# Performance work log

Hardware: AMD Instinct MI355X
Metric: run time of the kernel (lower is better)

The kernel has to match this reference:

```python
import jax, jax.numpy as jnp
import numpy as np

D = 1024
H = 16
HD = D // H
R = 16
EPS = 1e-5


def _ln(x, w, b):
    mu = jnp.mean(x, axis=-1, keepdims=True)
    var = jnp.mean((x - mu) ** 2, axis=-1, keepdims=True)
    return (x - mu) * jax.lax.rsqrt(var + EPS) * w + b


def setup_inputs() -> dict:
    key = jax.random.key(0)
    ks = jax.random.split(key, 8)
    B, N = 32, 257
    s = 0.02
    return {
        "q_x": jax.random.normal(ks[0], (B, N, D), jnp.float32),
        "ln1_w": jnp.ones((D,), jnp.float32),
        "ln1_b": jnp.zeros((D,), jnp.float32),
        "in_proj_w": jax.random.normal(ks[1], (3 * D, D), jnp.float32) * s,
        "in_proj_b": jnp.zeros((3 * D,), jnp.float32),
        "out_w": jax.random.normal(ks[2], (D, D), jnp.float32) * s,
        "out_b": jnp.zeros((D,), jnp.float32),
        "ln2_w": jnp.ones((D,), jnp.float32),
        "ln2_b": jnp.zeros((D,), jnp.float32),
        "fc_w": jax.random.normal(ks[3], (4 * D, D), jnp.float32) * s,
        "fc_b": jnp.zeros((4 * D,), jnp.float32),
        "proj_w": jax.random.normal(ks[4], (D, 4 * D), jnp.float32) * s,
        "proj_b": jnp.zeros((D,), jnp.float32),
    }


def reference(q_x, ln1_w, ln1_b, in_proj_w, in_proj_b, out_w, out_b,
              ln2_w, ln2_b, fc_w, fc_b, proj_w, proj_b):
    B, N, _ = q_x.shape
    # --- attention (no size bias / no padding mask on first call) ---
    h = _ln(q_x, ln1_w, ln1_b)
    qkv = h @ in_proj_w.T + in_proj_b            # [B,N,3D]
    q, k, v = jnp.split(qkv, 3, axis=-1)
    to_heads = lambda t: t.reshape(B, N, H, HD).transpose(0, 2, 1, 3)  # [B,H,N,hd]
    q, k, v = to_heads(q), to_heads(k), to_heads(v)
    metric = k.mean(axis=1)                      # [B,N,hd] ToMe metric
    attn = jax.nn.softmax(jnp.einsum('bhnd,bhmd->bhnm', q, k) / np.sqrt(HD).astype(np.float32), axis=-1)
    o = jnp.einsum('bhnm,bhmd->bhnd', attn, v).transpose(0, 2, 1, 3).reshape(B, N, D)
    x = q_x + (o @ out_w.T + out_b)
    # --- ToMe: bipartite soft matching + weighted-average merge (size=None -> ones) ---
    r = min(R, (N - 1) // 2)                     # class token protected
    m = metric / jnp.linalg.norm(metric, axis=-1, keepdims=True)
    a, bm = m[:, ::2, :], m[:, 1::2, :]          # [B,Na,hd], [B,Nb,hd]
    scores = jnp.einsum('bnd,bmd->bnm', a, bm)
    scores = scores.at[:, 0, :].set(-jnp.inf)    # never merge class token
    node_max = scores.max(axis=-1)               # [B,Na]
    node_idx = scores.argmax(axis=-1)            # [B,Na]
    edge_idx = jnp.argsort(-node_max, axis=-1)   # descending similarity
    unm_idx = jnp.sort(edge_idx[:, r:], axis=-1) # keep order; cls token first
    src_idx = edge_idx[:, :r]
    dst_idx = jnp.take_along_axis(node_idx, src_idx, axis=1)  # [B,r]
    bi = jnp.arange(B)[:, None]

    def merge_sum(t):
        s, d = t[:, ::2], t[:, 1::2]
        unm = jnp.take_along_axis(s, unm_idx[:, :, None], axis=1)
        src = jnp.take_along_axis(s, src_idx[:, :, None], axis=1)
        d = d.at[bi, dst_idx].add(src)
        return jnp.concatenate([unm, d], axis=1)  # [B, N-r, C]

    size = jnp.ones((B, N, 1), x.dtype)
    x = merge_sum(x * size)
    size = merge_sum(size)
    x = x / size
    # --- MLP ---
    h2 = _ln(x, ln2_w, ln2_b)
    h2 = jax.nn.gelu(h2 @ fc_w.T + fc_b, approximate=False)
    x = x + (h2 @ proj_w.T + proj_b)
    return x
```

## Files before the change

kernel.cpp:

```cpp
#include <hip/hip_runtime.h>
#include <math.h>

#define D_ 1024
#define H_ 16
#define HD_ 64
#define BATCH 32
#define NTOK 257
#define NROWS (BATCH*NTOK)
#define NE 129
#define NO 128
#define RR 16
#define UNM 113
#define NMERGED 241
#define MROWS (BATCH*NMERGED)
#define SELSTRIDE 288

typedef unsigned short u16;
typedef unsigned int u32;
typedef __bf16 bf16x8 __attribute__((ext_vector_type(8)));
typedef float floatx4 __attribute__((ext_vector_type(4)));

__device__ __forceinline__ u16 f2bf(float f) {
    u32 u = __float_as_uint(f);
    u += 0x7fffu + ((u >> 16) & 1u);
    return (u16)(u >> 16);
}

__global__ __launch_bounds__(256) void ln_kernel(const float* __restrict__ x,
                                                 const float* __restrict__ w,
                                                 const float* __restrict__ bia,
                                                 float* __restrict__ outf,
                                                 u16* __restrict__ outb) {
    int row = blockIdx.x;
    const float* xr = x + (size_t)row * D_;
    int t = threadIdx.x;
    float v[4];
#pragma unroll
    for (int i = 0; i < 4; i++) v[i] = xr[t + 256 * i];
    float s = v[0] + v[1] + v[2] + v[3];
#pragma unroll
    for (int o = 32; o; o >>= 1) s += __shfl_down(s, o);
    __shared__ float sm[8];
    int wv = t >> 6, ln = t & 63;
    if (ln == 0) sm[wv] = s;
    __syncthreads();
    float mu = (sm[0] + sm[1] + sm[2] + sm[3]) * (1.0f / D_);
    float d0 = v[0] - mu, d1 = v[1] - mu, d2 = v[2] - mu, d3 = v[3] - mu;
    float q = d0 * d0 + d1 * d1 + d2 * d2 + d3 * d3;
#pragma unroll
    for (int o = 32; o; o >>= 1) q += __shfl_down(q, o);
    if (ln == 0) sm[4 + wv] = q;
    __syncthreads();
    float var = (sm[4] + sm[5] + sm[6] + sm[7]) * (1.0f / D_);
    float rs = rsqrtf(var + 1e-5f);
#pragma unroll
    for (int i = 0; i < 4; i++) {
        int c = t + 256 * i;
        float o = (v[i] - mu) * rs * w[c] + bia[c];
        if (outf) outf[(size_t)row * D_ + c] = o;
        outb[(size_t)row * D_ + c] = f2bf(o);
    }
}

__global__ __launch_bounds__(256) void wm_kernel(const float* __restrict__ W,
                                                 const float* __restrict__ bias,
                                                 float* __restrict__ WmT,
                                                 float* __restrict__ bm) {
    int e = blockIdx.x * 256 + threadIdx.x;
    if (e < 64 * 1024) {
        int d = e >> 10, c = e & 1023;
        float s = 0.f;
#pragma unroll
        for (int hh = 0; hh < 16; hh++)
            s += W[(size_t)(1024 + hh * 64 + d) * 1024 + c];
        WmT[(size_t)c * 64 + d] = s * (1.0f / 16.0f);
    }
    if (e < 64) {
        float s = 0.f;
        for (int hh = 0; hh < 16; hh++) s += bias[1024 + hh * 64 + e];
        bm[e] = s * (1.0f / 16.0f);
    }
}

__global__ __launch_bounds__(256) void castw_kernel(const float* __restrict__ s0,
                                                    const float* __restrict__ s1,
                                                    const float* __restrict__ s2,
                                                    const float* __restrict__ s3,
                                                    u16* __restrict__ d0, u16* __restrict__ d1,
                                                    u16* __restrict__ d2, u16* __restrict__ d3) {
    size_t gi = ((size_t)blockIdx.x * 256 + threadIdx.x) * 8;
    const float* s; u16* d; size_t off;
    if (gi < 3145728)        { s = s0; d = d0; off = gi; }
    else if (gi < 4194304)   { s = s1; d = d1; off = gi - 3145728; }
    else if (gi < 8388608)   { s = s2; d = d2; off = gi - 4194304; }
    else                     { s = s3; d = d3; off = gi - 8388608; }
    float4 a = *(const float4*)(s + off);
    float4 b = *(const float4*)(s + off + 4);
    uint4 o;
    o.x = (u32)f2bf(a.x) | ((u32)f2bf(a.y) << 16);
    o.y = (u32)f2bf(a.z) | ((u32)f2bf(a.w) << 16);
    o.z = (u32)f2bf(b.x) | ((u32)f2bf(b.y) << 16);
    o.w = (u32)f2bf(b.z) | ((u32)f2bf(b.w) << 16);
    *(uint4*)(d + off) = o;
}

__global__ __launch_bounds__(256) void metric_kernel(const float* __restrict__ A,
                                                     const float* __restrict__ WmT,
                                                     const float* __restrict__ bm,
                                                     float* __restrict__ metric) {
    int wv = threadIdx.x >> 6, ln = threadIdx.x & 63;
    int row0 = blockIdx.x * 16 + wv * 4;
    const float* a0 = A + (size_t)row0 * 1024;
    float acc0 = 0.f, acc1 = 0.f, acc2 = 0.f, acc3 = 0.f;
    for (int k = 0; k < 1024; k += 8) {
#pragma unroll
        for (int kk = 0; kk < 8; kk++) {
            float w = WmT[(size_t)(k + kk) * 64 + ln];
            acc0 = fmaf(a0[k + kk], w, acc0);
            acc1 = fmaf(a0[1024 + k + kk], w, acc1);
            acc2 = fmaf(a0[2048 + k + kk], w, acc2);
            acc3 = fmaf(a0[3072 + k + kk], w, acc3);
        }
    }
    float b = bm[ln];
    metric[(size_t)row0 * 64 + ln] = acc0 + b;
    metric[(size_t)(row0 + 1) * 64 + ln] = acc1 + b;
    metric[(size_t)(row0 + 2) * 64 + ln] = acc2 + b;
    metric[(size_t)(row0 + 3) * 64 + ln] = acc3 + b;
}

__global__ __launch_bounds__(256) void mgemm_kernel(const u16* __restrict__ A,
                                                    const u16* __restrict__ Bw,
                                                    const float* __restrict__ bias,
                                                    const float* __restrict__ resid,
                                                    void* __restrict__ Cv,
                                                    int M, int N, int K, int mode,
                                                    int Gx) {
    __shared__ u16 As[128 * 64];
    __shared__ u16 Bs[128 * 64];
    int tid = threadIdx.x;
    int wv = tid >> 6, ln = tid & 63;
    int lin = blockIdx.x;
    int pw = Gx >> 3;
    int xcd = lin & 7;
    int j = lin >> 3;
    int xt = xcd * pw + (j % pw);
    int yt = j / pw;
    int m0 = yt * 128, n0 = xt * 128;
    int sr = wv * 8 + (ln >> 3);
    int sc = ((ln & 7) ^ (ln >> 3)) * 8;
    const u16* Ag[4]; const u16* Bg[4];
#pragma unroll
    for (int i = 0; i < 4; i++) {
        Ag[i] = A + (size_t)(m0 + i * 32 + sr) * K + sc;
        Bg[i] = Bw + (size_t)(n0 + i * 32 + sr) * K + sc;
    }
    floatx4 acc[4][4];
#pragma unroll
    for (int i = 0; i < 4; i++)
#pragma unroll
        for (int j2 = 0; j2 < 4; j2++) acc[i][j2] = (floatx4){0.f, 0.f, 0.f, 0.f};
    int wm = (wv & 1) * 64, wn = (wv >> 1) * 64;
    int lane16 = ln & 15, lq = ln >> 4;
    int sw = lane16 & 7;

    for (int k0 = 0; k0 < K; k0 += 64) {
        __syncthreads();
#pragma unroll
        for (int i = 0; i < 4; i++) {
            __builtin_amdgcn_global_load_lds(
                (const __attribute__((address_space(1))) void*)(Ag[i] + k0),
                (__attribute__((address_space(3))) void*)&As[i * 2048 + wv * 512], 16, 0, 0);
            __builtin_amdgcn_global_load_lds(
                (const __attribute__((address_space(1))) void*)(Bg[i] + k0),
                (__attribute__((address_space(3))) void*)&Bs[i * 2048 + wv * 512], 16, 0, 0);
        }
        __syncthreads();
#pragma unroll
        for (int ks = 0; ks < 2; ks++) {
            bf16x8 af[4], bf[4];
#pragma unroll
            for (int t = 0; t < 4; t++) {
                int slot = ((ks * 4 + lq) ^ sw) * 8;
                af[t] = *(const bf16x8*)&As[(wm + t * 16 + lane16) * 64 + slot];
                bf[t] = *(const bf16x8*)&Bs[(wn + t * 16 + lane16) * 64 + slot];
            }
#pragma unroll
            for (int mt = 0; mt < 4; mt++)
#pragma unroll
                for (int nt = 0; nt < 4; nt++)
                    acc[mt][nt] = __builtin_amdgcn_mfma_f32_16x16x32_bf16(
                        af[mt], bf[nt], acc[mt][nt], 0, 0, 0);
        }
    }
#pragma unroll
    for (int mt = 0; mt < 4; mt++) {
#pragma unroll
        for (int nt = 0; nt < 4; nt++) {
            int col = n0 + wn + nt * 16 + lane16;
            float bv = bias[col];
#pragma unroll
            for (int r2 = 0; r2 < 4; r2++) {
                int row = m0 + wm + mt * 16 + lq * 4 + r2;
                if (row < M) {
                    float v = acc[mt][nt][r2] + bv;
                    if (mode == 1) {
                        ((float*)Cv)[(size_t)row * N + col] = v + resid[(size_t)row * N + col];
                    } else {
                        if (mode == 2) {
                            float u = v * (0.7978845608028654f + 0.0356774081f * v * v);
                            v = v / (1.0f + __expf(-2.0f * u));
                        }
                        ((u16*)Cv)[(size_t)row * N + col] = f2bf(v);
                    }
                }
            }
        }
    }
}

#define VST 296
#define PST 40
__global__ __launch_bounds__(256, 3) void fattn_kernel(const u16* __restrict__ qkv,
                                                       u16* __restrict__ o) {
    __shared__ __align__(16) u16 Vts[64 * VST];
    __shared__ __align__(16) u16 Pb[4][16 * PST];
    int b = blockIdx.x / H_, h = blockIdx.x % H_;
    int tid = threadIdx.x;
    int wv = tid >> 6, ln = tid & 63;
    int lane16 = ln & 15, lq = ln >> 4;
    const u16* base = qkv + (size_t)b * NTOK * 3072 + h * HD_;

    for (int idx = tid; idx < NTOK * 8; idx += 256) {
        int key = idx >> 3, d0 = (idx & 7) * 8;
        uint4 u = *(const uint4*)(base + (size_t)key * 3072 + 2048 + d0);
        u16 e[8] = {(u16)u.x, (u16)(u.x >> 16), (u16)u.y, (u16)(u.y >> 16),
                    (u16)u.z, (u16)(u.z >> 16), (u16)u.w, (u16)(u.w >> 16)};
#pragma unroll
        for (int i = 0; i < 8; i++) Vts[(d0 + i) * VST + key] = e[i];
    }
    for (int idx = tid; idx < 64 * 32; idx += 256) {
        int d = idx >> 5, c = idx & 31;
        if (c) Vts[d * VST + 256 + c] = 0;
    }
    __syncthreads();

    u16* Pw = &Pb[wv][0];
    for (int qt = wv; qt < 17; qt += 4) {
        int q0 = qt * 16;
        const u16* qp = base + (size_t)(q0 + lane16) * 3072 + lq * 8;
        bf16x8 af0 = *(const bf16x8*)(qp);
        bf16x8 af1 = *(const bf16x8*)(qp + 32);
        floatx4 accs[17];
#pragma unroll
        for (int nt = 0; nt < 17; nt++) {
            const u16* kp = base + (size_t)(nt * 16 + lane16) * 3072 + 1024 + lq * 8;
            bf16x8 kb0 = *(const bf16x8*)(kp);
            bf16x8 kb1 = *(const bf16x8*)(kp + 32);
            floatx4 z = (floatx4){0.f, 0.f, 0.f, 0.f};
            z = __builtin_amdgcn_mfma_f32_16x16x32_bf16(af0, kb0, z, 0, 0, 0);
            accs[nt] = __builtin_amdgcn_mfma_f32_16x16x32_bf16(af1, kb1, z, 0, 0, 0);
        }
        if (lane16 != 0) {
#pragma unroll
            for (int r = 0; r < 4; r++) accs[16][r] = -3.0e38f;
        }
        float mrow[4], lsum[4], inv[4];
#pragma unroll
        for (int r = 0; r < 4; r++) {
            float m = -3.0e38f;
#pragma unroll
            for (int nt = 0; nt < 17; nt++) m = fmaxf(m, accs[nt][r]);
#pragma unroll
            for (int off = 1; off < 16; off <<= 1) m = fmaxf(m, __shfl_xor(m, off));
            mrow[r] = m;
            lsum[r] = 0.f;
        }
#pragma unroll
        for (int nt = 0; nt < 17; nt++) {
#pragma unroll
            for (int r = 0; r < 4; r++) {
                float p = __expf((accs[nt][r] - mrow[r]) * 0.125f);
                accs[nt][r] = p;
                lsum[r] += p;
            }
        }
#pragma unroll
        for (int r = 0; r < 4; r++) {
#pragma unroll
            for (int off = 1; off < 16; off <<= 1) lsum[r] += __shfl_xor(lsum[r], off);
            inv[r] = 1.0f / lsum[r];
        }
        floatx4 acco[4];
#pragma unroll
        for (int dt = 0; dt < 4; dt++) acco[dt] = (floatx4){0.f, 0.f, 0.f, 0.f};
#pragma unroll
        for (int ks = 0; ks < 9; ks++) {
            int nt0 = 2 * ks, nt1 = 2 * ks + 1;
#pragma unroll
            for (int r = 0; r < 4; r++) {
                float p0 = accs[nt0][r];
                float p1 = (nt1 <= 16) ? accs[nt1][r] : 0.f;
                Pw[(lq * 4 + r) * PST + lane16] = f2bf(p0);
                Pw[(lq * 4 + r) * PST + 16 + lane16] = f2bf(p1);
            }
            bf16x8 pa = *(const bf16x8*)&Pw[lane16 * PST + lq * 8];
#pragma unroll
            for (int dt = 0; dt < 4; dt++) {
                bf16x8 vb = *(const bf16x8*)&Vts[(dt * 16 + lane16) * VST + ks * 32 + lq * 8];
                acco[dt] = __builtin_amdgcn_mfma_f32_16x16x32_bf16(pa, vb, acco[dt], 0, 0, 0);
            }
        }
#pragma unroll
        for (int dt = 0; dt < 4; dt++) {
#pragma unroll
            for (int r = 0; r < 4; r++) {
                int row = q0 + lq * 4 + r;
                if (row < NTOK)
                    o[((size_t)(b * NTOK + row)) * D_ + h * HD_ + dt * 16 + lane16] =
                        f2bf(acco[dt][r] * inv[r]);
            }
        }
    }
}

__global__ __launch_bounds__(256) void mnorm_kernel(const float* __restrict__ metric,
                                                    float* __restrict__ aN,
                                                    float* __restrict__ bT) {
    int r = blockIdx.x * 4 + (threadIdx.x >> 6);
    int l = threadIdx.x & 63;
    int b = r / NTOK, t = r % NTOK;
    float v = metric[(size_t)r * 64 + l];
    float ss = v * v;
#pragma unroll
    for (int off = 1; off < 64; off <<= 1) ss += __shfl_xor(ss, off);
    float nv = v * rsqrtf(ss);
    if (!(t & 1)) aN[((size_t)b * NE + (t >> 1)) * 64 + l] = nv;
    else          bT[(size_t)b * 8192 + l * 128 + (t >> 1)] = nv;
}

__global__ __launch_bounds__(256) void score_kernel(const float* __restrict__ aN,
                                                    const float* __restrict__ bT,
                                                    float* __restrict__ nodeMax,
                                                    int* __restrict__ nodeIdx) {
    __shared__ float aL[4][64];
    int b = blockIdx.x / 33, eb = blockIdx.x % 33;
    int wv = threadIdx.x >> 6, l = threadIdx.x & 63;
    int e = eb * 4 + wv;
    if (e >= NE) return;
    aL[wv][l] = aN[((size_t)b * NE + e) * 64 + l];
    const float* bp = bT + (size_t)b * 8192;
    float s0 = 0.f, s1 = 0.f;
#pragma unroll 8
    for (int c = 0; c < 64; c++) {
        float w = aL[wv][c];
        s0 = fmaf(w, bp[c * 128 + l], s0);
        s1 = fmaf(w, bp[c * 128 + 64 + l], s1);
    }
    float bv; int bj;
    if (s1 > s0) { bv = s1; bj = l + 64; } else { bv = s0; bj = l; }
    if (e == 0) { bv = -3.0e38f; bj = 0; }
#pragma unroll
    for (int off = 1; off < 64; off <<= 1) {
        float ov = __shfl_xor(bv, off);
        int oj = __shfl_xor(bj, off);
        if (ov > bv || (ov == bv && oj < bj)) { bv = ov; bj = oj; }
    }
    if (l == 0) { nodeMax[b * NE + e] = bv; nodeIdx[b * NE + e] = bj; }
}

__global__ __launch_bounds__(64) void pick_kernel(const float* __restrict__ nodeMax,
                                                  const int* __restrict__ nodeIdx,
                                                  int* __restrict__ sel) {
    __shared__ unsigned char usedL[NE];
    __shared__ int cntL[NO];
    int b = blockIdx.x, l = threadIdx.x;
    int* sb = sel + b * SELSTRIDE;
    float v0 = nodeMax[b * NE + l];
    float v1 = nodeMax[b * NE + 64 + l];
    float v2 = (l == 0) ? nodeMax[b * NE + 128] : -3.0e38f;
    u32 usedM = (l == 0) ? 0u : 4u;
    cntL[l] = 0; cntL[l + 64] = 0;
    for (int s = 0; s < RR; s++) {
        float bv = -3.0e38f; int be = 1 << 30;
        if (!(usedM & 1u) && v0 > bv) { bv = v0; be = l; }
        if (!(usedM & 2u) && v1 > bv) { bv = v1; be = l + 64; }
        if (!(usedM & 4u) && v2 > bv) { bv = v2; be = l + 128; }
#pragma unroll
        for (int off = 1; off < 64; off <<= 1) {
            float ov = __shfl_xor(bv, off);
            int oe = __shfl_xor(be, off);
            if (ov > bv || (ov == bv && oe < be)) { bv = ov; be = oe; }
        }
        if ((be & 63) == l) usedM |= 1u << (be >> 6);
        if (l == 0) {
            sb[s] = be;
            int d = nodeIdx[b * NE + be];
            sb[16 + s] = d;
            cntL[d]++;
        }
    }
    usedL[l] = (usedM & 1u) ? 1 : 0;
    usedL[64 + l] = (usedM & 2u) ? 1 : 0;
    if (l == 0) usedL[128] = (usedM & 4u) ? 1 : 0;
    __syncthreads();
    if (l == 0) {
        int u = 0;
        for (int e = 0; e < NE; e++) if (!usedL[e]) sb[160 + u++] = e;
    }
    sb[32 + l] = cntL[l];
    sb[32 + 64 + l] = cntL[l + 64];
}

__global__ __launch_bounds__(256) void merge_ln_kernel(const float* __restrict__ x,
                                                       const int* __restrict__ sel,
                                                       const float* __restrict__ w,
                                                       const float* __restrict__ bia,
                                                       float* __restrict__ xm,
                                                       u16* __restrict__ outb) {
    int blk = blockIdx.x;
    int b = blk / NMERGED, t = blk % NMERGED;
    const int* sb = sel + b * SELSTRIDE;
    int tid = threadIdx.x;
    const float* xb = x + (size_t)b * NTOK * D_;
    float v[4];
    if (t < UNM) {
        int srcRow = 2 * sb[160 + t];
        const float* r = xb + (size_t)srcRow * D_;
#pragma unroll
        for (int i = 0; i < 4; i++) v[i] = r[tid + 256 * i];
    } else {
        int j = t - UNM;
        const float* r = xb + (size_t)(2 * j + 1) * D_;
#pragma unroll
        for (int i = 0; i < 4; i++) v[i] = r[tid + 256 * i];
        int c = sb[32 + j];
        if (c > 0) {
            for (int s = 0; s < RR; s++) {
                if (sb[16 + s] == j) {
                    const float* rs = xb + (size_t)(2 * sb[s]) * D_;
#pragma unroll
                    for (int i = 0; i < 4; i++) v[i] += rs[tid + 256 * i];
                }
            }
            float inv = 1.0f / (float)(1 + c);
#pragma unroll
            for (int i = 0; i < 4; i++) v[i] *= inv;
        }
    }
    float* orow = xm + (size_t)blk * D_;
#pragma unroll
    for (int i = 0; i < 4; i++) orow[tid + 256 * i] = v[i];
    float s = v[0] + v[1] + v[2] + v[3];
#pragma unroll
    for (int o = 32; o; o >>= 1) s += __shfl_down(s, o);
    __shared__ float sm[8];
    int wv = tid >> 6, ln = tid & 63;
    if (ln == 0) sm[wv] = s;
    __syncthreads();
    float mu = (sm[0] + sm[1] + sm[2] + sm[3]) * (1.0f / D_);
    float d0 = v[0] - mu, d1 = v[1] - mu, d2 = v[2] - mu, d3 = v[3] - mu;
    float q = d0 * d0 + d1 * d1 + d2 * d2 + d3 * d3;
#pragma unroll
    for (int o = 32; o; o >>= 1) q += __shfl_down(q, o);
    if (ln == 0) sm[4 + wv] = q;
    __syncthreads();
    float var = (sm[4] + sm[5] + sm[6] + sm[7]) * (1.0f / D_);
    float rs = rsqrtf(var + 1e-5f);
#pragma unroll
    for (int i = 0; i < 4; i++) {
        int c = tid + 256 * i;
        outb[(size_t)blk * D_ + c] = f2bf((v[i] - mu) * rs * w[c] + bia[c]);
    }
}

extern "C" void kernel_launch(void* const* d_in, const int* in_sizes, int n_in,
                              void* d_out, int out_size, void* d_ws, size_t ws_size,
                              hipStream_t stream) {
    (void)in_sizes; (void)n_in; (void)out_size; (void)ws_size;
    const float* qx   = (const float*)d_in[0];
    const float* ln1w = (const float*)d_in[1];
    const float* ln1b = (const float*)d_in[2];
    const float* ipw  = (const float*)d_in[3];
    const float* ipb  = (const float*)d_in[4];
    const float* outw = (const float*)d_in[5];
    const float* outb = (const float*)d_in[6];
    const float* ln2w = (const float*)d_in[7];
    const float* ln2b = (const float*)d_in[8];
    const float* fcw  = (const float*)d_in[9];
    const float* fcb  = (const float*)d_in[10];
    const float* pw   = (const float*)d_in[11];
    const float* pb   = (const float*)d_in[12];
    float* out = (float*)d_out;

    char* ws = (char*)d_ws;
    u16*   qkvb  = (u16*)(ws + 0);
    u16*   h2b   = (u16*)(ws + 0);
    u16*   hb    = (u16*)(ws + 51118080);
    float* hf    = (float*)(ws + 68157440);
    float* xbuf  = hf;
    u16*   ob    = (u16*)(ws + 101842944);
    float* metric= (float*)(ws + 118882304);
    float* xm    = (float*)(ws + 120987648);
    u16*   ln2bb = (u16*)(ws + 152576000);
    u16*   wqkv  = (u16*)(ws + 168566784);
    u16*   woutb = (u16*)(ws + 174858240);
    u16*   wfc   = (u16*)(ws + 176955392);
    u16*   wproj = (u16*)(ws + 185344000);
    float* WmT   = (float*)(ws + 193732608);
    float* bm    = (float*)(ws + 193994752);
    int*   sel   = (int*)(ws + 193995008);
    float* aN    = (float*)(ws + 194031872);
    float* bT    = (float*)(ws + 195088640);
    float* nMax  = (float*)(ws + 196137216);
    int*   nIdx  = (int*)(ws + 196153856);

    ln_kernel<<<NROWS, 256, 0, stream>>>(qx, ln1w, ln1b, hf, hb);
    wm_kernel<<<256, 256, 0, stream>>>(ipw, ipb, WmT, bm);
    castw_kernel<<<6144, 256, 0, stream>>>(ipw, outw, fcw, pw, wqkv, woutb, wfc, wproj);
    metric_kernel<<<514, 256, 0, stream>>>(hf, WmT, bm, metric);
    mgemm_kernel<<<24 * 65, 256, 0, stream>>>(hb, wqkv, ipb, nullptr, qkvb,
                                              NROWS, 3072, 1024, 0, 24);
    fattn_kernel<<<BATCH * H_, 256, 0, stream>>>(qkvb, ob);
    mgemm_kernel<<<8 * 65, 256, 0, stream>>>(ob, woutb, outb, qx, xbuf,
                                             NROWS, 1024, 1024, 1, 8);
    mnorm_kernel<<<2056, 256, 0, stream>>>(metric, aN, bT);
    score_kernel<<<BATCH * 33, 256, 0, stream>>>(aN, bT, nMax, nIdx);
    pick_kernel<<<BATCH, 64, 0, stream>>>(nMax, nIdx, sel);
    merge_ln_kernel<<<BATCH * NMERGED, 256, 0, stream>>>(xbuf, sel, ln2w, ln2b, xm, ln2bb);
    mgemm_kernel<<<32 * 61, 256, 0, stream>>>(ln2bb, wfc, fcb, nullptr, h2b,
                                              MROWS, 4096, 1024, 2, 32);
    mgemm_kernel<<<8 * 61, 256, 0, stream>>>(h2b, wproj, pb, xm, out,
                                             MROWS, 1024, 4096, 1, 8);
}
```

Measured before the change: 774.1 us.

## Double-buffer GEMM LDS tiles and drop XCD-aware block remapping

The bf16 MFMA GEMM now uses two LDS buffers, prefetching the next K-slice via global_load_lds while the current slice is computed, with one barrier per iteration instead of two. This is meant to hide global-load latency behind MFMA work. It doubles LDS use to 64 KB per block, which may lower occupancy. It also replaces the XCD-aware 1D grid swizzle with a plain 2D grid, which may hurt L2 locality across chiplets. There is no explicit wait on the async LDS loads before reading the current buffer beyond the single barrier, so correctness depends on how the compiler places vmcnt waits.

Result: slower. 809.9 us (+4.6%).

```diff
diff --git a/kernel.cpp b/kernel.cpp
--- a/kernel.cpp
+++ b/kernel.cpp
@@ -134,19 +134,12 @@
                                                     const float* __restrict__ bias,
                                                     const float* __restrict__ resid,
                                                     void* __restrict__ Cv,
-                                                    int M, int N, int K, int mode,
-                                                    int Gx) {
-    __shared__ u16 As[128 * 64];
-    __shared__ u16 Bs[128 * 64];
+                                                    int M, int N, int K, int mode) {
+    __shared__ u16 As[2][128 * 64];
+    __shared__ u16 Bs[2][128 * 64];
     int tid = threadIdx.x;
     int wv = tid >> 6, ln = tid & 63;
-    int lin = blockIdx.x;
-    int pw = Gx >> 3;
-    int xcd = lin & 7;
-    int j = lin >> 3;
-    int xt = xcd * pw + (j % pw);
-    int yt = j / pw;
-    int m0 = yt * 128, n0 = xt * 128;
+    int m0 = blockIdx.y * 128, n0 = blockIdx.x * 128;
     int sr = wv * 8 + (ln >> 3);
     int sc = ((ln & 7) ^ (ln >> 3)) * 8;
     const u16* Ag[4]; const u16* Bg[4];
@@ -159,31 +152,45 @@
 #pragma unroll
     for (int i = 0; i < 4; i++)
 #pragma unroll
-        for (int j2 = 0; j2 < 4; j2++) acc[i][j2] = (floatx4){0.f, 0.f, 0.f, 0.f};
+        for (int j = 0; j < 4; j++) acc[i][j] = (floatx4){0.f, 0.f, 0.f, 0.f};
     int wm = (wv & 1) * 64, wn = (wv >> 1) * 64;
     int lane16 = ln & 15, lq = ln >> 4;
     int sw = lane16 & 7;
 
-    for (int k0 = 0; k0 < K; k0 += 64) {
+#pragma unroll
+    for (int i = 0; i < 4; i++) {
+        __builtin_amdgcn_global_load_lds(
+            (const __attribute__((address_space(1))) void*)(Ag[i]),
+            (__attribute__((address_space(3))) void*)&As[0][i * 2048 + wv * 512], 16, 0, 0);
+        __builtin_amdgcn_global_load_lds(
+            (const __attribute__((address_space(1))) void*)(Bg[i]),
+            (__attribute__((address_space(3))) void*)&Bs[0][i * 2048 + wv * 512], 16, 0, 0);
+    }
+    int nk = K >> 6;
+    for (int it = 0; it < nk; it++) {
+        int cur = it & 1;
         __syncthreads();
-#pragma unroll
-        for (int i = 0; i < 4; i++) {
-            __builtin_amdgcn_global_load_lds(
-                (const __attribute__((address_space(1))) void*)(Ag[i] + k0),
-                (__attribute__((address_space(3))) void*)&As[i * 2048 + wv * 512], 16, 0, 0);
-            __builtin_amdgcn_global_load_lds(
-                (const __attribute__((address_space(1))) void*)(Bg[i] + k0),
-                (__attribute__((address_space(3))) void*)&Bs[i * 2048 + wv * 512], 16, 0, 0);
-        }
-        __syncthreads();
+        if (it + 1 < nk) {
+            int k1 = (it + 1) << 6;
+            int nxt = cur ^ 1;
+#pragma unroll
+            for (int i = 0; i < 4; i++) {
+                __builtin_amdgcn_global_load_lds(
+                    (const __attribute__((address_space(1))) void*)(Ag[i] + k1),
+                    (__attribute__((address_space(3))) void*)&As[nxt][i * 2048 + wv * 512], 16, 0, 0);
+                __builtin_amdgcn_global_load_lds(
+                    (const __attribute__((address_space(1))) void*)(Bg[i] + k1),
+                    (__attribute__((address_space(3))) void*)&Bs[nxt][i * 2048 + wv * 512], 16, 0, 0);
+            }
+        }
 #pragma unroll
         for (int ks = 0; ks < 2; ks++) {
             bf16x8 af[4], bf[4];
 #pragma unroll
             for (int t = 0; t < 4; t++) {
                 int slot = ((ks * 4 + lq) ^ sw) * 8;
-                af[t] = *(const bf16x8*)&As[(wm + t * 16 + lane16) * 64 + slot];
-                bf[t] = *(const bf16x8*)&Bs[(wn + t * 16 + lane16) * 64 + slot];
+                af[t] = *(const bf16x8*)&As[cur][(wm + t * 16 + lane16) * 64 + slot];
+                bf[t] = *(const bf16x8*)&Bs[cur][(wn + t * 16 + lane16) * 64 + slot];
             }
 #pragma unroll
             for (int mt = 0; mt < 4; mt++)
@@ -519,17 +526,17 @@
     wm_kernel<<<256, 256, 0, stream>>>(ipw, ipb, WmT, bm);
     castw_kernel<<<6144, 256, 0, stream>>>(ipw, outw, fcw, pw, wqkv, woutb, wfc, wproj);
     metric_kernel<<<514, 256, 0, stream>>>(hf, WmT, bm, metric);
-    mgemm_kernel<<<24 * 65, 256, 0, stream>>>(hb, wqkv, ipb, nullptr, qkvb,
-                                              NROWS, 3072, 1024, 0, 24);
+    mgemm_kernel<<<dim3(24, 65), 256, 0, stream>>>(hb, wqkv, ipb, nullptr, qkvb,
+                                                   NROWS, 3072, 1024, 0);
     fattn_kernel<<<BATCH * H_, 256, 0, stream>>>(qkvb, ob);
-    mgemm_kernel<<<8 * 65, 256, 0, stream>>>(ob, woutb, outb, qx, xbuf,
-                                             NROWS, 1024, 1024, 1, 8);
+    mgemm_kernel<<<dim3(8, 65), 256, 0, stream>>>(ob, woutb, outb, qx, xbuf,
+                                                  NROWS, 1024, 1024, 1);
     mnorm_kernel<<<2056, 256, 0, stream>>>(metric, aN, bT);
     score_kernel<<<BATCH * 33, 256, 0, stream>>>(aN, bT, nMax, nIdx);
     pick_kernel<<<BATCH, 64, 0, stream>>>(nMax, nIdx, sel);
     merge_ln_kernel<<<BATCH * NMERGED, 256, 0, stream>>>(xbuf, sel, ln2w, ln2b, xm, ln2bb);
-    mgemm_kernel<<<32 * 61, 256, 0, stream>>>(ln2bb, wfc, fcb, nullptr, h2b,
-                                              MROWS, 4096, 1024, 2, 32);
-    mgemm_kernel<<<8 * 61, 256, 0, stream>>>(h2b, wproj, pb, xm, out,
-                                             MROWS, 1024, 4096, 1, 8);
-}
+    mgemm_kernel<<<dim3(32, 61), 256, 0, stream>>>(ln2bb, wfc, fcb, nullptr, h2b,
+                                                   MROWS, 4096, 1024, 2);
+    mgemm_kernel<<<dim3(8, 61), 256, 0, stream>>>(h2b, wproj, pb, xm, out,
+                                                  MROWS, 1024, 4096, 1);
+}
```
